# Kernel tuning notes

Hardware: AMD Instinct MI355X
Metric: run time of the kernel (lower is better)

## Reference

```python
import jax, jax.numpy as jnp
import numpy as np

N, D_DIM, K, R = 100000, 256, 4, 16
E_RAND = 1600000
ETA, LAM, C = 0.5, 0.1, 0.5


def setup_inputs() -> dict:
    key = jax.random.key(0)
    k1, k2, k3, k4 = jax.random.split(key, 4)
    Z = jax.random.normal(k1, (N, D_DIM), jnp.float32)
    U = jax.random.normal(k2, (K, D_DIM, R), jnp.float32) / np.float32(np.sqrt(D_DIM))
    Dmat = jax.random.normal(k3, (D_DIM, D_DIM), jnp.float32) / np.float32(np.sqrt(D_DIM))
    head_w = jnp.ones((K,), jnp.float32) / K
    rnd = jax.random.randint(k4, (2, E_RAND), 0, N)
    loops = jnp.stack([jnp.arange(N), jnp.arange(N)])  # self-loops: every node has an in-edge
    edge_index = jnp.concatenate([rnd, loops], axis=1)  # [2, E]
    return {"Z": Z, "U": U, "Dmat": Dmat, "head_w": head_w, "edge_index": edge_index}


def reference(Z, U, Dmat, head_w, edge_index):
    src, dst = edge_index[0], edge_index[1]
    scale = np.float32(np.sqrt(R))

    # Project into all K subspaces at once: [K, n, r]
    ZU = jnp.einsum('nd,kdr->knr', Z, U)
    zs = ZU[:, src, :]                      # [K, E, r] gather at src
    zd = ZU[:, dst, :]                      # [K, E, r] gather at dst
    logits = (zs * zd).sum(-1) / scale      # [K, E]

    seg_max = jax.vmap(lambda l: jax.ops.segment_max(l, dst, num_segments=N))(logits)
    exp_l = jnp.exp(logits - seg_max[:, dst])
    seg_sum = jax.vmap(lambda e: jax.ops.segment_sum(e, dst, num_segments=N))(exp_l)
    alpha = exp_l / (seg_sum[:, dst] + 1e-16)  # [K, E]

    weighted = alpha[..., None] * zs           # [K, E, r]
    agg = jax.vmap(lambda w_: jax.ops.segment_sum(w_, dst, num_segments=N))(weighted)  # [K, n, r]

    w = jax.nn.softmax(head_w)
    ssa = jnp.einsum('k,knr,kdr->nd', w, agg, U)  # sum_k w_k * (agg_k @ U_k^T)

    Z_half = (1.0 - C) * Z + C * ssa

    # ISTA step (matches torch code exactly):
    DZ = Z_half @ Dmat.T
    residual = Z_half - DZ @ Dmat
    grad_step = Z_half + ETA * (residual @ Dmat)
    return jax.nn.relu(grad_step - ETA * LAM)
```

## Files before the change

### kernel.cpp

```cpp
#include <hip/hip_runtime.h>
#include <stdint.h>


typedef unsigned short u16;
typedef unsigned int u32;
typedef __attribute__((ext_vector_type(8))) short bf16x8;
typedef __attribute__((ext_vector_type(4))) float f32x4;

#define PB 256

__device__ __forceinline__ u16 f2bf(float f) {
    u32 u = __float_as_uint(f);
    u32 r = u + 0x7fffu + ((u >> 16) & 1u);
    return (u16)(r >> 16);
}
__device__ __forceinline__ float bl(u32 p) { return __uint_as_float(p << 16); }
__device__ __forceinline__ float bh(u32 p) { return __uint_as_float(p & 0xffff0000u); }

__device__ __forceinline__ void gload_lds16(const void* g, void* l) {
    __builtin_amdgcn_global_load_lds(
        (const __attribute__((address_space(1))) void*)g,
        (__attribute__((address_space(3))) void*)l, 16, 0, 0);
}

__global__ void k_prep1(const float* __restrict__ D, float* __restrict__ G) {
    int i = blockIdx.x, j = threadIdx.x;
    float acc = 0.f;
    for (int d = 0; d < 256; ++d)
        acc += D[d * 256 + i] * D[d * 256 + j];
    G[i * 256 + j] = acc;
}

__global__ void k_prep2(const float* __restrict__ D, const float* __restrict__ G,
                        float* __restrict__ A) {
    int t = blockIdx.x, j = threadIdx.x;
    float acc = 0.f;
    for (int u = 0; u < 256; ++u)
        acc += G[t * 256 + u] * D[u * 256 + j];
    A[t * 256 + j] = 0.5f * (D[t * 256 + j] - acc) + (t == j ? 1.f : 0.f);
}

__global__ void k_prep3(const float* __restrict__ A, u16* __restrict__ Bt) {
    int c = blockIdx.x, k = threadIdx.x;
    Bt[c * 320 + k] = f2bf(0.5f * A[k * 256 + c]);
}

__global__ void k_prep4(const float* __restrict__ U, const float* __restrict__ A,
                        u16* __restrict__ Bt) {
    int j = blockIdx.x, c = threadIdx.x;
    int k = j >> 4, r = j & 15;
    float acc = 0.f;
    for (int d = 0; d < 256; ++d)
        acc += U[k * 4096 + d * 16 + r] * A[d * 256 + c];
    Bt[c * 320 + 256 + j] = f2bf(0.5f * acc);
}

__global__ void k_prep5(const float* __restrict__ U, u16* __restrict__ U2t) {
    int j = blockIdx.x, d = threadIdx.x;
    U2t[j * 256 + d] = f2bf(U[(j >> 4) * 4096 + d * 16 + (j & 15)]);
}

__global__ __launch_bounds__(256) void k_cnt1(const int* __restrict__ ei,
                                              int* __restrict__ cnt2, int E, int nbuck) {
    __shared__ int h[512];
    int t = threadIdx.x, b = blockIdx.x;
    for (int i = t; i < nbuck; i += 256) h[i] = 0;
    __syncthreads();
    int per = (E + PB - 1) / PB;
    int lo = b * per;
    int hi = lo + per; if (hi > E) hi = E;
    for (int e = lo + t; e < hi; e += 256)
        atomicAdd(&h[ei[E + e] >> 8], 1);
    __syncthreads();
    for (int i = t; i < nbuck; i += 256)
        cnt2[b * nbuck + i] = h[i];
}

__global__ __launch_bounds__(256) void k_cscan1(const int* __restrict__ cnt2,
                                                int* __restrict__ pre2,
                                                int* __restrict__ tot, int nbuck) {
    __shared__ int s[256];
    int t = threadIdx.x, b = blockIdx.x;
    int v = cnt2[t * nbuck + b];
    s[t] = v;
    __syncthreads();
    for (int o = 1; o < 256; o <<= 1) {
        int x = (t >= o) ? s[t - o] : 0;
        __syncthreads();
        s[t] += x;
        __syncthreads();
    }
    pre2[t * nbuck + b] = s[t] - v;
    if (t == 255) tot[b] = s[255];
}

__global__ __launch_bounds__(512) void k_cscan2(const int* __restrict__ tot,
                                                int* __restrict__ bbase, int nbuck) {
    __shared__ int s[512];
    int t = threadIdx.x;
    int v = (t < nbuck) ? tot[t] : 0;
    s[t] = v;
    __syncthreads();
    for (int o = 1; o < 512; o <<= 1) {
        int x = (t >= o) ? s[t - o] : 0;
        __syncthreads();
        s[t] += x;
        __syncthreads();
    }
    if (t < nbuck) bbase[t] = s[t] - v;
}

__global__ __launch_bounds__(256) void k_place(const int* __restrict__ ei,
                                               const int* __restrict__ pre2,
                                               const int* __restrict__ bbase,
                                               int* __restrict__ part, int E, int nbuck) {
    __shared__ int baseS[512];
    __shared__ int cur[512];
    int t = threadIdx.x, b = blockIdx.x;
    for (int i = t; i < nbuck; i += 256) {
        baseS[i] = bbase[i] + pre2[b * nbuck + i];
        cur[i] = 0;
    }
    __syncthreads();
    int per = (E + PB - 1) / PB;
    int lo = b * per;
    int hi = lo + per; if (hi > E) hi = E;
    for (int e = lo + t; e < hi; e += 256) {
        int s = ei[e];
        int d = ei[E + e];
        int bk = d >> 8;
        int r = atomicAdd(&cur[bk], 1);
        part[baseS[bk] + r] = (s << 8) | (d & 255);
    }
}

__global__ __launch_bounds__(256) void k_bucket(const int* __restrict__ part,
                                                const int* __restrict__ tot,
                                                const int* __restrict__ bbase,
                                                int* __restrict__ off,
                                                int* __restrict__ cnt,
                                                int* __restrict__ esrc, int n) {
    __shared__ int ncnt[256], excl[256], cur[256], sc[256];
    int t = threadIdx.x, b = blockIdx.x;
    ncnt[t] = 0;
    cur[t] = 0;
    __syncthreads();
    int base = bbase[b], m = tot[b];
    for (int i = t; i < m; i += 256)
        atomicAdd(&ncnt[part[base + i] & 255], 1);
    __syncthreads();
    int v = ncnt[t];
    sc[t] = v;
    __syncthreads();
    for (int o = 1; o < 256; o <<= 1) {
        int x = (t >= o) ? sc[t - o] : 0;
        __syncthreads();
        sc[t] += x;
        __syncthreads();
    }
    excl[t] = sc[t] - v;
    int node = b * 256 + t;
    if (node < n) {
        off[node] = base + excl[t];
        cnt[node] = v;
    }
    __syncthreads();
    for (int i = t; i < m; i += 256) {
        int pk = part[base + i];
        int j = pk & 255;
        int r = atomicAdd(&cur[j], 1);
        esrc[base + excl[j] + r] = pk >> 8;
    }
}

__global__ __launch_bounds__(256, 4) void k_zumm(const float* __restrict__ Z,
                                                 const u16* __restrict__ U2t,
                                                 u16* __restrict__ ZUb,
                                                 u16* __restrict__ Zb, int n) {
    const int t = threadIdx.x;
    const int w = t >> 6;
    const int lane = t & 63;
    const int m16 = lane & 15;
    const int quad = lane >> 4;
    const int nb = blockIdx.x * 64;
    const int row = nb + w * 16 + m16;
    const int rowc = row < n ? row : n - 1;
    const float* zr = Z + (size_t)rowc * 256 + quad * 8;

    float4 zf0[8], zf1[8];
#pragma unroll
    for (int ks = 0; ks < 8; ++ks) {
        zf0[ks] = *reinterpret_cast<const float4*>(zr + ks * 32);
        zf1[ks] = *reinterpret_cast<const float4*>(zr + ks * 32 + 4);
    }
    __builtin_amdgcn_sched_barrier(0);

    uint4 pk[8];
#pragma unroll
    for (int ks = 0; ks < 8; ++ks) {
        pk[ks].x = (u32)f2bf(zf0[ks].x) | ((u32)f2bf(zf0[ks].y) << 16);
        pk[ks].y = (u32)f2bf(zf0[ks].z) | ((u32)f2bf(zf0[ks].w) << 16);
        pk[ks].z = (u32)f2bf(zf1[ks].x) | ((u32)f2bf(zf1[ks].y) << 16);
        pk[ks].w = (u32)f2bf(zf1[ks].z) | ((u32)f2bf(zf1[ks].w) << 16);
    }
    __builtin_amdgcn_sched_barrier(0);

    f32x4 acc[4];
#pragma unroll
    for (int nt = 0; nt < 4; ++nt) acc[nt] = (f32x4){0.f, 0.f, 0.f, 0.f};
#pragma unroll
    for (int ks = 0; ks < 8; ++ks) {
        bf16x8 a;
        __builtin_memcpy(&a, &pk[ks], 16);
#pragma unroll
        for (int nt = 0; nt < 4; ++nt) {
            bf16x8 b = *reinterpret_cast<const bf16x8*>(
                U2t + (size_t)(nt * 16 + m16) * 256 + ks * 32 + quad * 8);
            acc[nt] = __builtin_amdgcn_mfma_f32_16x16x32_bf16(a, b, acc[nt], 0, 0, 0);
        }
    }
    __builtin_amdgcn_sched_barrier(0);

    if (row < n) {
#pragma unroll
        for (int ks = 0; ks < 8; ++ks)
            *reinterpret_cast<uint4*>(Zb + (size_t)row * 256 + ks * 32 + quad * 8) = pk[ks];
    }
#pragma unroll
    for (int r = 0; r < 4; ++r) {
        int node = nb + w * 16 + quad * 4 + r;
        if (node < n) {
#pragma unroll
            for (int nt = 0; nt < 4; ++nt)
                ZUb[(size_t)node * 64 + nt * 16 + m16] = f2bf(acc[nt][r]);
        }
    }
}

__global__ __launch_bounds__(256) void k_agg(const u16* __restrict__ ZUb,
                                             const int* __restrict__ esrc,
                                             const int* __restrict__ off,
                                             const int* __restrict__ cnt,
                                             const float* __restrict__ hwp,
                                             u16* __restrict__ Vb, int n) {
    int node = blockIdx.x * 4 + (threadIdx.x >> 6);
    int lane = threadIdx.x & 63;
    if (node >= n) return;
    const int q = lane & 15;
    const int g = lane >> 4;
    uint2 zdp = *reinterpret_cast<const uint2*>(ZUb + (size_t)node * 64 + q * 4);
    float zd0 = bl(zdp.x), zd1 = bh(zdp.x), zd2 = bl(zdp.y), zd3 = bh(zdp.y);
    int base = off[node];
    int deg = cnt[node];

    int s0 = (g < deg) ? esrc[base + g] : 0;
    int s1 = (4 + g < deg) ? esrc[base + 4 + g] : 0;
    uint2 z0 = *reinterpret_cast<const uint2*>(ZUb + (size_t)s0 * 64 + q * 4);

    float ax = 0.f, ay = 0.f, az = 0.f, aw = 0.f, ssum = 0.f;
    for (int c0 = 0; c0 < deg; c0 += 4) {
        int e2 = c0 + 8 + g;
        int s2 = (e2 < deg) ? esrc[base + e2] : 0;
        uint2 z1 = *reinterpret_cast<const uint2*>(
            ZUb + (size_t)s1 * 64 + q * 4);
        bool valid = (c0 + g) < deg;
        float v0 = bl(z0.x), v1 = bh(z0.x), v2 = bl(z0.y), v3 = bh(z0.y);
        float p = v0 * zd0 + v1 * zd1 + v2 * zd2 + v3 * zd3;
        p += __shfl_xor(p, 1);
        p += __shfl_xor(p, 2);
        float ew = valid ? __expf(p * 0.25f) : 0.f;
        ax += ew * v0; ay += ew * v1;
        az += ew * v2; aw += ew * v3;
        ssum += ew;
        s1 = s2; z0 = z1;
    }
    ax += __shfl_xor(ax, 16); ax += __shfl_xor(ax, 32);
    ay += __shfl_xor(ay, 16); ay += __shfl_xor(ay, 32);
    az += __shfl_xor(az, 16); az += __shfl_xor(az, 32);
    aw += __shfl_xor(aw, 16); aw += __shfl_xor(aw, 32);
    ssum += __shfl_xor(ssum, 16); ssum += __shfl_xor(ssum, 32);

    if (g == 0) {
        float h0 = hwp[0], h1 = hwp[1], h2 = hwp[2], h3 = hwp[3];
        float mx = fmaxf(fmaxf(h0, h1), fmaxf(h2, h3));
        float e0 = __expf(h0 - mx), e1 = __expf(h1 - mx),
              e2 = __expf(h2 - mx), e3 = __expf(h3 - mx);
        float es = e0 + e1 + e2 + e3;
        int hd = q >> 2;
        float wk = (hd == 0 ? e0 : hd == 1 ? e1 : hd == 2 ? e2 : e3) / es;
        float inv = wk / ssum;
        uint2 pk;
        pk.x = (u32)f2bf(ax * inv) | ((u32)f2bf(ay * inv) << 16);
        pk.y = (u32)f2bf(az * inv) | ((u32)f2bf(aw * inv) << 16);
        *reinterpret_cast<uint2*>(&Vb[(size_t)node * 64 + q * 4]) = pk;
    }
}

__global__ __launch_bounds__(256, 4) void k_out(const u16* __restrict__ Zb,
                                                const u16* __restrict__ Vb,
                                                const u16* __restrict__ Bt,
                                                float* __restrict__ out, int n) {
    __shared__ __align__(16) u16 sA[64 * 256];
    __shared__ __align__(16) u16 sV[64 * 64];
    const int t = threadIdx.x;
    const int w = t >> 6;
    const int lane = t & 63;
    const int m16 = lane & 15;
    const int quad = lane >> 4;
    const int nb = blockIdx.x * 64;

#pragma unroll
    for (int i = 0; i < 8; ++i) {
        int c = i * 256 + w * 64 + lane;
        int row = c >> 5, col = c & 31;
        int scol = col ^ (row & 7);
        int gr = nb + row; if (gr >= n) gr = n - 1;
        gload_lds16(Zb + (size_t)gr * 256 + scol * 8,
                    sA + (size_t)(i * 256 + w * 64) * 8);
    }
#pragma unroll
    for (int i = 0; i < 2; ++i) {
        int c = i * 256 + w * 64 + lane;
        int row = c >> 3, col = c & 7;
        int scol = col ^ (row & 7);
        int gr = nb + row; if (gr >= n) gr = n - 1;
        gload_lds16(Vb + (size_t)gr * 64 + scol * 8,
                    sV + (size_t)(i * 256 + w * 64) * 8);
    }
    __syncthreads();

    f32x4 acc[4][4];
#pragma unroll
    for (int mt = 0; mt < 4; ++mt)
#pragma unroll
        for (int nt = 0; nt < 4; ++nt)
            acc[mt][nt] = (f32x4){0.f, 0.f, 0.f, 0.f};

    const u16* bbase4[4];
#pragma unroll
    for (int nt = 0; nt < 4; ++nt)
        bbase4[nt] = Bt + (size_t)(w * 64 + nt * 16 + m16) * 320 + quad * 8;

    const u32 asw = (u32)(m16 & 7) << 4;

    for (int ks = 0; ks < 8; ++ks) {
        bf16x8 a[4], b[4];
#pragma unroll
        for (int mt = 0; mt < 4; ++mt)
            a[mt] = *reinterpret_cast<const bf16x8*>(
                (char*)sA + (u32)(mt * 16 + m16) * 512 +
                (((u32)(ks * 64 + quad * 16)) ^ asw));
#pragma unroll
        for (int nt = 0; nt < 4; ++nt)
            b[nt] = *reinterpret_cast<const bf16x8*>(bbase4[nt] + ks * 32);
#pragma unroll
        for (int mt = 0; mt < 4; ++mt)
#pragma unroll
            for (int nt = 0; nt < 4; ++nt)
                acc[mt][nt] = __builtin_amdgcn_mfma_f32_16x16x32_bf16(
                    a[mt], b[nt], acc[mt][nt], 0, 0, 0);
    }
#pragma unroll
    for (int ks = 8; ks < 10; ++ks) {
        bf16x8 a[4], b[4];
#pragma unroll
        for (int mt = 0; mt < 4; ++mt)
            a[mt] = *reinterpret_cast<const bf16x8*>(
                (char*)sV + (u32)(mt * 16 + m16) * 128 +
                (((u32)((ks - 8) * 64 + quad * 16)) ^ asw));
#pragma unroll
        for (int nt = 0; nt < 4; ++nt)
            b[nt] = *reinterpret_cast<const bf16x8*>(bbase4[nt] + ks * 32);
#pragma unroll
        for (int mt = 0; mt < 4; ++mt)
#pragma unroll
            for (int nt = 0; nt < 4; ++nt)
                acc[mt][nt] = __builtin_amdgcn_mfma_f32_16x16x32_bf16(
                    a[mt], b[nt], acc[mt][nt], 0, 0, 0);
    }

#pragma unroll
    for (int mt = 0; mt < 4; ++mt) {
#pragma unroll
        for (int r = 0; r < 4; ++r) {
            int row = nb + mt * 16 + quad * 4 + r;
            if (row < n) {
#pragma unroll
                for (int nt = 0; nt < 4; ++nt) {
                    int col = w * 64 + nt * 16 + m16;
                    out[(size_t)row * 256 + col] =
                        fmaxf(acc[mt][nt][r] - 0.05f, 0.f);
                }
            }
        }
    }
}

extern "C" void kernel_launch(void* const* d_in, const int* in_sizes, int n_in,
                              void* d_out, int out_size, void* d_ws, size_t ws_size,
                              hipStream_t stream) {
    const float* Z  = (const float*)d_in[0];
    const float* U  = (const float*)d_in[1];
    const float* Dm = (const float*)d_in[2];
    const float* hw = (const float*)d_in[3];
    const int*   ei = (const int*)d_in[4];
    const int n = in_sizes[0] / 256;
    const int E = in_sizes[4] / 2;
    float* out = (float*)d_out;
    const int nbuck = (n + 255) >> 8;

    char* wp = (char*)d_ws;
    u16* ZUb    = (u16*)wp;
    u16* Zb     = (u16*)(wp + (size_t)n * 128);
    int* part   = (int*)Zb;
    int* cnt2   = part + E;
    int* pre2   = cnt2 + PB * nbuck;
    u16* Vb     = Zb + (size_t)n * 256;
    float* G    = (float*)(Vb + (size_t)n * 64);
    float* A    = G + 65536;
    u16* Bt     = (u16*)(A + 65536);
    u16* U2t    = Bt + 256 * 320;
    int* esrc   = (int*)(U2t + 64 * 256);
    int* off    = esrc + E;
    int* cnt    = off + n;
    int* tot    = cnt + n;
    int* bbase  = tot + nbuck;

    k_prep1<<<256, 256, 0, stream>>>(Dm, G);
    k_prep2<<<256, 256, 0, stream>>>(Dm, G, A);
    k_prep3<<<256, 256, 0, stream>>>(A, Bt);
    k_prep4<<<64, 256, 0, stream>>>(U, A, Bt);
    k_prep5<<<64, 256, 0, stream>>>(U, U2t);

    k_cnt1<<<PB, 256, 0, stream>>>(ei, cnt2, E, nbuck);
    k_cscan1<<<nbuck, 256, 0, stream>>>(cnt2, pre2, tot, nbuck);
    k_cscan2<<<1, 512, 0, stream>>>(tot, bbase, nbuck);
    k_place<<<PB, 256, 0, stream>>>(ei, pre2, bbase, part, E, nbuck);
    k_bucket<<<nbuck, 256, 0, stream>>>(part, tot, bbase, off, cnt, esrc, n);

    k_zumm<<<(n + 63) / 64, 256, 0, stream>>>(Z, U2t, ZUb, Zb, n);
    k_agg<<<(n + 3) / 4, 256, 0, stream>>>(ZUb, esrc, off, cnt, hw, Vb, n);
    k_out<<<(n + 63) / 64, 256, 0, stream>>>(Zb, Vb, Bt, out, n);
}
```

Measured before the change: 419.9 us.

## Permute K dimension for coalesced Z loads and vectorize prep GEMV kernels

Reorders the reduction dimension inside each 32-wide chunk so each lane's two float4 loads of Z in k_zumm are 64 bytes apart and contiguous across the quad, rather than 32 bytes apart with a stride. The weight matrices U2t and Bt's first 256 rows are built with the matching permutation so the results stay correct. The small prep kernels for D^T D, A and U·A are also rewritten so each thread computes four outputs with float4 loads using 64-thread blocks. The aim is better load coalescing on the big Z read and fewer scalar loads in setup. The risk is that the permutation has to line up exactly with how the k_out MFMA consumes Zb.

```diff
diff --git a/kernel.cpp b/kernel.cpp
--- a/kernel.cpp
+++ b/kernel.cpp
@@ -17,47 +17,72 @@
 __device__ __forceinline__ float bl(u32 p) { return __uint_as_float(p << 16); }
 __device__ __forceinline__ float bh(u32 p) { return __uint_as_float(p & 0xffff0000u); }
 
+__device__ __forceinline__ int kperm(int dm) {
+    int rr = dm & 31, q = rr >> 3, j = rr & 7;
+    return (dm & ~31) + (j < 4 ? q * 4 + j : 16 + q * 4 + (j - 4));
+}
+
 __device__ __forceinline__ void gload_lds16(const void* g, void* l) {
     __builtin_amdgcn_global_load_lds(
         (const __attribute__((address_space(1))) void*)g,
         (__attribute__((address_space(3))) void*)l, 16, 0, 0);
 }
 
-__global__ void k_prep1(const float* __restrict__ D, float* __restrict__ G) {
-    int i = blockIdx.x, j = threadIdx.x;
-    float acc = 0.f;
-    for (int d = 0; d < 256; ++d)
-        acc += D[d * 256 + i] * D[d * 256 + j];
-    G[i * 256 + j] = acc;
-}
-
-__global__ void k_prep2(const float* __restrict__ D, const float* __restrict__ G,
-                        float* __restrict__ A) {
-    int t = blockIdx.x, j = threadIdx.x;
-    float acc = 0.f;
-    for (int u = 0; u < 256; ++u)
-        acc += G[t * 256 + u] * D[u * 256 + j];
-    A[t * 256 + j] = 0.5f * (D[t * 256 + j] - acc) + (t == j ? 1.f : 0.f);
+__global__ __launch_bounds__(64) void k_prep1(const float* __restrict__ D, float* __restrict__ G) {
+    int i = blockIdx.x, j0 = threadIdx.x * 4;
+    float4 acc = {0.f, 0.f, 0.f, 0.f};
+    for (int d = 0; d < 256; ++d) {
+        float s = D[d * 256 + i];
+        float4 b = *reinterpret_cast<const float4*>(D + d * 256 + j0);
+        acc.x += s * b.x; acc.y += s * b.y; acc.z += s * b.z; acc.w += s * b.w;
+    }
+    *reinterpret_cast<float4*>(G + i * 256 + j0) = acc;
+}
+
+__global__ __launch_bounds__(64) void k_prep2(const float* __restrict__ D, const float* __restrict__ G,
+                                              float* __restrict__ A) {
+    int tR = blockIdx.x, j0 = threadIdx.x * 4;
+    float4 acc = {0.f, 0.f, 0.f, 0.f};
+    for (int u = 0; u < 256; ++u) {
+        float s = G[tR * 256 + u];
+        float4 b = *reinterpret_cast<const float4*>(D + u * 256 + j0);
+        acc.x += s * b.x; acc.y += s * b.y; acc.z += s * b.z; acc.w += s * b.w;
+    }
+    float4 dv = *reinterpret_cast<const float4*>(D + tR * 256 + j0);
+    float4 o;
+    o.x = 0.5f * (dv.x - acc.x) + (tR == j0 + 0 ? 1.f : 0.f);
+    o.y = 0.5f * (dv.y - acc.y) + (tR == j0 + 1 ? 1.f : 0.f);
+    o.z = 0.5f * (dv.z - acc.z) + (tR == j0 + 2 ? 1.f : 0.f);
+    o.w = 0.5f * (dv.w - acc.w) + (tR == j0 + 3 ? 1.f : 0.f);
+    *reinterpret_cast<float4*>(A + tR * 256 + j0) = o;
 }
 
 __global__ void k_prep3(const float* __restrict__ A, u16* __restrict__ Bt) {
     int c = blockIdx.x, k = threadIdx.x;
-    Bt[c * 320 + k] = f2bf(0.5f * A[k * 256 + c]);
-}
-
-__global__ void k_prep4(const float* __restrict__ U, const float* __restrict__ A,
-                        u16* __restrict__ Bt) {
-    int j = blockIdx.x, c = threadIdx.x;
+    Bt[c * 320 + k] = f2bf(0.5f * A[kperm(k) * 256 + c]);
+}
+
+__global__ __launch_bounds__(64) void k_prep4(const float* __restrict__ U, const float* __restrict__ A,
+                                              u16* __restrict__ Bt) {
+    int j = blockIdx.x;
     int k = j >> 4, r = j & 15;
-    float acc = 0.f;
-    for (int d = 0; d < 256; ++d)
-        acc += U[k * 4096 + d * 16 + r] * A[d * 256 + c];
-    Bt[c * 320 + 256 + j] = f2bf(0.5f * acc);
+    int c0 = threadIdx.x * 4;
+    float4 acc = {0.f, 0.f, 0.f, 0.f};
+    for (int d = 0; d < 256; ++d) {
+        float s = U[k * 4096 + d * 16 + r];
+        float4 b = *reinterpret_cast<const float4*>(A + d * 256 + c0);
+        acc.x += s * b.x; acc.y += s * b.y; acc.z += s * b.z; acc.w += s * b.w;
+    }
+    Bt[(c0 + 0) * 320 + 256 + j] = f2bf(0.5f * acc.x);
+    Bt[(c0 + 1) * 320 + 256 + j] = f2bf(0.5f * acc.y);
+    Bt[(c0 + 2) * 320 + 256 + j] = f2bf(0.5f * acc.z);
+    Bt[(c0 + 3) * 320 + 256 + j] = f2bf(0.5f * acc.w);
 }
 
 __global__ void k_prep5(const float* __restrict__ U, u16* __restrict__ U2t) {
     int j = blockIdx.x, d = threadIdx.x;
-    U2t[j * 256 + d] = f2bf(U[(j >> 4) * 4096 + d * 16 + (j & 15)]);
+    int dz = kperm(d);
+    U2t[j * 256 + d] = f2bf(U[(j >> 4) * 4096 + dz * 16 + (j & 15)]);
 }
 
 __global__ __launch_bounds__(256) void k_cnt1(const int* __restrict__ ei,
@@ -185,13 +210,13 @@
     const int nb = blockIdx.x * 64;
     const int row = nb + w * 16 + m16;
     const int rowc = row < n ? row : n - 1;
-    const float* zr = Z + (size_t)rowc * 256 + quad * 8;
+    const char* zrow = (const char*)(Z + (size_t)rowc * 256);
 
     float4 zf0[8], zf1[8];
 #pragma unroll
     for (int ks = 0; ks < 8; ++ks) {
-        zf0[ks] = *reinterpret_cast<const float4*>(zr + ks * 32);
-        zf1[ks] = *reinterpret_cast<const float4*>(zr + ks * 32 + 4);
+        zf0[ks] = *reinterpret_cast<const float4*>(zrow + ks * 128 + quad * 16);
+        zf1[ks] = *reinterpret_cast<const float4*>(zrow + ks * 128 + 64 + quad * 16);
     }
     __builtin_amdgcn_sched_barrier(0);
 
@@ -426,10 +451,10 @@
     int* tot    = cnt + n;
     int* bbase  = tot + nbuck;
 
-    k_prep1<<<256, 256, 0, stream>>>(Dm, G);
-    k_prep2<<<256, 256, 0, stream>>>(Dm, G, A);
+    k_prep1<<<256, 64, 0, stream>>>(Dm, G);
+    k_prep2<<<256, 64, 0, stream>>>(Dm, G, A);
     k_prep3<<<256, 256, 0, stream>>>(A, Bt);
-    k_prep4<<<64, 256, 0, stream>>>(U, A, Bt);
+    k_prep4<<<64, 64, 0, stream>>>(U, A, Bt);
     k_prep5<<<64, 256, 0, stream>>>(U, U2t);
 
     k_cnt1<<<PB, 256, 0, stream>>>(ei, cnt2, E, nbuck);
```

Result: no change. 427.9 us (+1.9%).

## Drop bf16 Z intermediate; convert fp32 Z in output kernel with permuted K order

Applied to the files above, without the earlier changes.

Stops k_zumm from writing a bf16 copy of Z. k_out now loads fp32 Z directly, converts it to bf16 and stores it swizzled into LDS. To keep the fp32 loads contiguous, the K dimension is permuted, and the prep kernels permute the Dmat- and U-derived weights to match. This saves the write and re-read of the bf16 intermediate but doubles the bytes k_out reads for Z and replaces the async global-to-LDS loads with register round trips.

```diff
diff --git a/kernel.cpp b/kernel.cpp
--- a/kernel.cpp
+++ b/kernel.cpp
@@ -16,6 +16,11 @@
 }
 __device__ __forceinline__ float bl(u32 p) { return __uint_as_float(p << 16); }
 __device__ __forceinline__ float bh(u32 p) { return __uint_as_float(p & 0xffff0000u); }
+
+__device__ __forceinline__ int kperm(int dm) {
+    int rr = dm & 31, q = rr >> 3, j = rr & 7;
+    return (dm & ~31) + (j < 4 ? q * 4 + j : 16 + q * 4 + (j - 4));
+}
 
 __device__ __forceinline__ void gload_lds16(const void* g, void* l) {
     __builtin_amdgcn_global_load_lds(
@@ -42,7 +47,7 @@
 
 __global__ void k_prep3(const float* __restrict__ A, u16* __restrict__ Bt) {
     int c = blockIdx.x, k = threadIdx.x;
-    Bt[c * 320 + k] = f2bf(0.5f * A[k * 256 + c]);
+    Bt[c * 320 + k] = f2bf(0.5f * A[kperm(k) * 256 + c]);
 }
 
 __global__ void k_prep4(const float* __restrict__ U, const float* __restrict__ A,
@@ -57,7 +62,8 @@
 
 __global__ void k_prep5(const float* __restrict__ U, u16* __restrict__ U2t) {
     int j = blockIdx.x, d = threadIdx.x;
-    U2t[j * 256 + d] = f2bf(U[(j >> 4) * 4096 + d * 16 + (j & 15)]);
+    int dz = kperm(d);
+    U2t[j * 256 + d] = f2bf(U[(j >> 4) * 4096 + dz * 16 + (j & 15)]);
 }
 
 __global__ __launch_bounds__(256) void k_cnt1(const int* __restrict__ ei,
@@ -175,8 +181,7 @@
 
 __global__ __launch_bounds__(256, 4) void k_zumm(const float* __restrict__ Z,
                                                  const u16* __restrict__ U2t,
-                                                 u16* __restrict__ ZUb,
-                                                 u16* __restrict__ Zb, int n) {
+                                                 u16* __restrict__ ZUb, int n) {
     const int t = threadIdx.x;
     const int w = t >> 6;
     const int lane = t & 63;
@@ -185,13 +190,13 @@
     const int nb = blockIdx.x * 64;
     const int row = nb + w * 16 + m16;
     const int rowc = row < n ? row : n - 1;
-    const float* zr = Z + (size_t)rowc * 256 + quad * 8;
+    const char* zrow = (const char*)(Z + (size_t)rowc * 256);
 
     float4 zf0[8], zf1[8];
 #pragma unroll
     for (int ks = 0; ks < 8; ++ks) {
-        zf0[ks] = *reinterpret_cast<const float4*>(zr + ks * 32);
-        zf1[ks] = *reinterpret_cast<const float4*>(zr + ks * 32 + 4);
+        zf0[ks] = *reinterpret_cast<const float4*>(zrow + ks * 128 + quad * 16);
+        zf1[ks] = *reinterpret_cast<const float4*>(zrow + ks * 128 + 64 + quad * 16);
     }
     __builtin_amdgcn_sched_barrier(0);
 
@@ -221,11 +226,6 @@
     }
     __builtin_amdgcn_sched_barrier(0);
 
-    if (row < n) {
-#pragma unroll
-        for (int ks = 0; ks < 8; ++ks)
-            *reinterpret_cast<uint4*>(Zb + (size_t)row * 256 + ks * 32 + quad * 8) = pk[ks];
-    }
 #pragma unroll
     for (int r = 0; r < 4; ++r) {
         int node = nb + w * 16 + quad * 4 + r;
@@ -296,7 +296,7 @@
     }
 }
 
-__global__ __launch_bounds__(256, 4) void k_out(const u16* __restrict__ Zb,
+__global__ __launch_bounds__(256, 4) void k_out(const float* __restrict__ Z,
                                                 const u16* __restrict__ Vb,
                                                 const u16* __restrict__ Bt,
                                                 float* __restrict__ out, int n) {
@@ -310,15 +310,6 @@
     const int nb = blockIdx.x * 64;
 
 #pragma unroll
-    for (int i = 0; i < 8; ++i) {
-        int c = i * 256 + w * 64 + lane;
-        int row = c >> 5, col = c & 31;
-        int scol = col ^ (row & 7);
-        int gr = nb + row; if (gr >= n) gr = n - 1;
-        gload_lds16(Zb + (size_t)gr * 256 + scol * 8,
-                    sA + (size_t)(i * 256 + w * 64) * 8);
-    }
-#pragma unroll
     for (int i = 0; i < 2; ++i) {
         int c = i * 256 + w * 64 + lane;
         int row = c >> 3, col = c & 7;
@@ -326,6 +317,23 @@
         int gr = nb + row; if (gr >= n) gr = n - 1;
         gload_lds16(Vb + (size_t)gr * 64 + scol * 8,
                     sV + (size_t)(i * 256 + w * 64) * 8);
+    }
+
+#pragma unroll
+    for (int i = 0; i < 8; ++i) {
+        int c = i * 256 + t;
+        int row = c >> 5, col = c & 31;
+        int ks = col >> 2, q = col & 3;
+        int gr = nb + row; if (gr >= n) gr = n - 1;
+        const char* zrow = (const char*)(Z + (size_t)gr * 256);
+        float4 a0 = *reinterpret_cast<const float4*>(zrow + ks * 128 + q * 16);
+        float4 a1 = *reinterpret_cast<const float4*>(zrow + ks * 128 + 64 + q * 16);
+        uint4 pk;
+        pk.x = (u32)f2bf(a0.x) | ((u32)f2bf(a0.y) << 16);
+        pk.y = (u32)f2bf(a0.z) | ((u32)f2bf(a0.w) << 16);
+        pk.z = (u32)f2bf(a1.x) | ((u32)f2bf(a1.y) << 16);
+        pk.w = (u32)f2bf(a1.z) | ((u32)f2bf(a1.w) << 16);
+        *reinterpret_cast<uint4*>((char*)sA + row * 512 + ((col ^ (row & 7)) << 4)) = pk;
     }
     __syncthreads();
 
@@ -438,7 +446,7 @@
     k_place<<<PB, 256, 0, stream>>>(ei, pre2, bbase, part, E, nbuck);
     k_bucket<<<nbuck, 256, 0, stream>>>(part, tot, bbase, off, cnt, esrc, n);
 
-    k_zumm<<<(n + 63) / 64, 256, 0, stream>>>(Z, U2t, ZUb, Zb, n);
+    k_zumm<<<(n + 63) / 64, 256, 0, stream>>>(Z, U2t, ZUb, n);
     k_agg<<<(n + 3) / 4, 256, 0, stream>>>(ZUb, esrc, off, cnt, hw, Vb, n);
-    k_out<<<(n + 63) / 64, 256, 0, stream>>>(Zb, Vb, Bt, out, n);
-}
+    k_out<<<(n + 63) / 64, 256, 0, stream>>>(Z, Vb, Bt, out, n);
+}
```

Measured after the change: 419.1 us. No clear change (-0.2%).
